# Optimization experiments

Hardware: AMD Instinct MI355X
Metric: run time of the kernel (lower is better)

## Reference

```python
import jax, jax.numpy as jnp
import numpy as np

INPUT_DIM = 10
SIG_DEPTH = 3
HIDDEN = 64
D_AUG = INPUT_DIM + 1  # time augmentation
LOGSIG_DIM = min(sum(D_AUG ** k // max(1, k) for k in range(1, SIG_DEPTH + 1)), 512)  # = 512
B, N = 1024, 256


def _compute_logsigs(features):
    """Vectorized computation of the per-step prefix-path signature features.

    For prefix length k+1 the torch code time-augments with linspace(0,1,k+1),
    i.e. dt = 1/k, which makes the time-related signature terms k-dependent.
    All terms reduce to cumulative sums over t, computed once for all k.
    Returns (B, N, LOGSIG_DIM); row k=0 is zeros (torch uses zeros at k=0).
    """
    Bsz, n, D = features.shape
    d = D + 1  # augmented dim (time first)
    dtype = features.dtype
    x0 = features[:, :1, :]
    inc = features[:, 1:, :] - features[:, :-1, :]          # (B, n-1, D) feature increments
    rel = features - x0                                      # x_t - x_0, (B, n, D)
    t_idx = jnp.arange(n - 1, dtype=dtype)
    # A[k-1] = sum_{t<k} t * dx_t   (time-row of level-2 term, before dt scaling)
    A = jnp.cumsum(t_idx[None, :, None] * inc, axis=1)       # (B, n-1, D)
    # Bc[k-1] = sum_{t=0}^{k-1} (x_t - x_0)   (time-column, before dt scaling)
    Bc = jnp.cumsum(rel[:, :-1, :], axis=1)                  # (B, n-1, D)
    # C[k-1] = sum_{t<k} (x_t - x_0) outer dx_t  (feature-feature level-2 block)
    C = jnp.cumsum(rel[:, :-1, :, None] * inc[:, :, None, :], axis=1)  # (B, n-1, D, D)
    ks = jnp.arange(1, n, dtype=dtype)                       # k = 1..n-1
    inv_k = 1.0 / ks
    tt = 0.5 * (ks - 1) * inv_k                              # sum t*dt^2 = (k-1)/(2k)
    # level-1: [T=1, x_k - x_0]
    sig1 = jnp.concatenate([jnp.ones((Bsz, n - 1, 1), dtype), rel[:, 1:, :]], axis=-1)  # (B, n-1, d)
    # level-2 matrix, augmented order [time, features]
    sig2 = jnp.zeros((Bsz, n - 1, d, d), dtype)
    sig2 = sig2.at[:, :, 0, 0].set(tt[None, :])
    sig2 = sig2.at[:, :, 0, 1:].set(inv_k[None, :, None] * A)
    sig2 = sig2.at[:, :, 1:, 0].set(inv_k[None, :, None] * Bc)
    sig2 = sig2.at[:, :, 1:, 1:].set(C)
    sig2f = sig2.reshape(Bsz, n - 1, d * d)
    # level-3 (torch: flatten(sig1 outer sig2_flat), truncated); only build needed rows
    sig3_len = LOGSIG_DIM - d - d * d                        # 512 - 11 - 121 = 380
    rows = (sig3_len + d * d - 1) // (d * d)                 # 4 rows of sig1 suffice
    sig3 = (sig1[..., :rows, None] * sig2f[..., None, :]).reshape(Bsz, n - 1, rows * d * d)[..., :sig3_len]
    logsig = jnp.concatenate([sig1, sig2f, sig3], axis=-1)[..., :LOGSIG_DIM]  # (B, n-1, 512)
    return jnp.concatenate([jnp.zeros((Bsz, 1, LOGSIG_DIM), dtype), logsig], axis=1)


def setup_inputs() -> dict:
    key = jax.random.key(0)
    k0, k1, k2, k3 = jax.random.split(key, 4)
    features = jax.random.normal(k0, (B, N, INPUT_DIM), jnp.float32)
    in_dim = LOGSIG_DIM + INPUT_DIM + 1  # 523
    W1 = jax.random.normal(k1, (in_dim, HIDDEN), jnp.float32) / np.sqrt(in_dim)
    b1 = jnp.zeros((HIDDEN,), jnp.float32)
    W2 = jax.random.normal(k2, (HIDDEN, HIDDEN), jnp.float32) / np.sqrt(HIDDEN)
    b2 = jnp.zeros((HIDDEN,), jnp.float32)
    W3 = jax.random.normal(k3, (HIDDEN, 1), jnp.float32) / np.sqrt(HIDDEN)
    b3 = jnp.zeros((1,), jnp.float32)
    return {"features": features, "W1": W1, "b1": b1, "W2": W2, "b2": b2, "W3": W3, "b3": b3}


def reference(features, W1, b1, W2, b2, W3, b3):
    logsigs = _compute_logsigs(features)  # (B, N, LOGSIG_DIM)
    Bsz = features.shape[0]

    def step(prev_delta, inputs):
        ls, ft = inputs  # (B, L), (B, D)
        x = jnp.concatenate([ls, ft, prev_delta], axis=-1)
        h = jax.nn.relu(x @ W1 + b1)
        h = jax.nn.relu(h @ W2 + b2)
        delta = h @ W3 + b3  # (B, 1)
        return delta, delta[:, 0]

    ls_t = jnp.swapaxes(logsigs, 0, 1)   # (N, B, L)
    ft_t = jnp.swapaxes(features, 0, 1)  # (N, B, D)
    _, deltas = jax.lax.scan(step, jnp.zeros((Bsz, 1), features.dtype), (ls_t, ft_t))
    return jnp.swapaxes(deltas, 0, 1)    # (B, N)
```

## Files before the change

### kernel.cpp

```cpp
#include <hip/hip_runtime.h>

#define NB 1024
#define NT 256
#define IND 10
#define HID 64

#define KSTEPS 14
#define XS 456
#define WMF_HALVES (KSTEPS * 4 * 64 * 8)

typedef short bf16x8 __attribute__((ext_vector_type(8)));
typedef float f32x4 __attribute__((ext_vector_type(4)));

__device__ __forceinline__ int qmap(int kk) {
    if (kk < 10) return 1 + kk;
    if (kk < 20) return 11 * (kk - 10 + 1);
    int i = (kk - 20) / 10, c = (kk - 20) % 10;
    return 11 * (i + 1) + 1 + c;
}

__device__ __forceinline__ unsigned bf16rne(float x) {
    unsigned u = __float_as_uint(x);
    return (u + 0x7fffu + ((u >> 16) & 1u)) >> 16;
}
__device__ __forceinline__ unsigned pk2(float a, float b) {
    return bf16rne(a) | (bf16rne(b) << 16);
}

__device__ float wm_value(int kk, int j, const float* __restrict__ W1,
                          const float* __restrict__ b1) {
    if (kk < 384) {
        int sec = kk >> 7;
        int rem = kk & 127;
        int w = rem >> 5, i = rem & 31;
        if (i >= 30) return 0.f;
        int q = qmap(30 * w + i);
        if (sec == 0) return W1[(11 + q) * 64 + j] + W1[(132 + q) * 64 + j];
        if (sec == 1) return W1[(253 + q) * 64 + j];
        return W1[(374 + q) * 64 + j];
    }
    if (kk < 400) {
        int i = kk - 384;
        if (i < 10) return W1[(496 + i) * 64 + j];
        if (i == 10) return W1[506 * 64 + j];
        return W1[(507 + (i - 11)) * 64 + j];
    }
    if (kk < 410) return W1[(1 + (kk - 400)) * 64 + j];
    if (kk < 420) return W1[(512 + (kk - 410)) * 64 + j];
    if (kk == 420) return W1[11 * 64 + j] + W1[132 * 64 + j];
    if (kk == 421) return W1[253 * 64 + j];
    if (kk == 422) return W1[374 * 64 + j];
    if (kk == 423) return W1[495 * 64 + j];
    if (kk == 424) return W1[0 * 64 + j];
    if (kk == 425) return b1[j];
    return 0.f;
}

__global__ void pack_mfma_kernel(const float* __restrict__ W1,
                                 const float* __restrict__ b1,
                                 unsigned short* __restrict__ Wmf) {
    int idx = blockIdx.x * 256 + threadIdx.x;
    if (idx >= WMF_HALVES) return;
    int half = idx & 7;
    int lane = (idx >> 3) & 63;
    int rec = idx >> 9;
    int s = rec >> 2, jb = rec & 3;
    int kk = 32 * s + (lane >> 4) * 8 + half;
    int j = 16 * jb + (lane & 15);
    Wmf[idx] = (unsigned short)bf16rne(wm_value(kk, j, W1, b1));
}

__global__ __launch_bounds__(256, 1) void presig9_kernel(
    const float* __restrict__ features, const unsigned short* __restrict__ Wmf,
    float* __restrict__ pre1) {
    const int b = blockIdx.x;
    const int tid = threadIdx.x;
    const int l = tid & 63;
    const int wu = tid >> 6;

    __shared__ __align__(16) float sF[NT * IND];
    __shared__ __align__(16) unsigned short sX[64 * XS];
    __shared__ float sBase[128];

    {
        const float4* src = (const float4*)(features + b * (NT * IND));
        float4* dst = (float4*)sF;
        for (int e = tid; e < NT * IND / 4; e += 256) dst[e] = src[e];
    }
    float f0[IND];
#pragma unroll
    for (int c = 0; c < IND; ++c) f0[c] = features[b * (NT * IND) + c];

    if (tid < 128) sBase[tid] = 0.f;
    __syncthreads();

    for (int tile = 0; tile < 4; ++tile) {
        const int t0 = tile * 64;

        const int r = t0 + l;
        float rf = (float)r;
        float fr[IND], rel[IND], inc[IND];
#pragma unroll
        for (int c = 0; c < IND; ++c) fr[c] = sF[r * IND + c];
#pragma unroll
        for (int c = 0; c < IND; ++c) rel[c] = fr[c] - f0[c];
        {
            bool last = (r >= NT - 1);
#pragma unroll
            for (int c = 0; c < IND; ++c)
                inc[c] = last ? 0.f : (sF[(r + 1) * IND + c] - fr[c]);
        }
        float p[30], own[30];
        if (wu == 0) {
#pragma unroll
            for (int c = 0; c < 10; ++c) p[c] = rf * inc[c];
#pragma unroll
            for (int i = 0; i < 10; ++i) p[10 + i] = rel[i];
#pragma unroll
            for (int c = 0; c < 10; ++c) p[20 + c] = rel[0] * inc[c];
        } else {
            const int i0 = 3 * wu - 2;
#pragma unroll
            for (int q = 0; q < 30; ++q) {
                int i = i0 + q / 10, c = q % 10;
                p[q] = rel[i] * inc[c];
            }
        }
#pragma unroll
        for (int i = 0; i < 30; ++i) own[i] = p[i];
#pragma unroll
        for (int dsh = 0; dsh < 6; ++dsh) {
            const int d = 1 << dsh;
            bool ok = (l >= d);
#pragma unroll
            for (int i = 0; i < 30; ++i) {
                float v = __shfl_up(p[i], d, 64);
                if (ok) p[i] += v;
            }
        }
        float inv_r = (r > 0) ? 1.f / rf : 0.f;
        float v[30];
#pragma unroll
        for (int i = 0; i < 30; ++i) {
            float x = sBase[wu * 32 + i] + p[i] - own[i];
            if (wu == 0 && i < 20) x *= inv_r;
            v[i] = x;
        }

        {
            float g0 = rel[0], g1 = rel[1];
            uint4* xr = (uint4*)&sX[l * XS];
            uint4* x0 = (uint4*)&sX[l * XS + 128];
            uint4* x1 = (uint4*)&sX[l * XS + 256];
            int qb = 8 * wu;
#pragma unroll
            for (int q = 0; q < 3; ++q) {
                uint4 tr, t0v, t1v;
                tr.x = pk2(v[8*q+0], v[8*q+1]); tr.y = pk2(v[8*q+2], v[8*q+3]);
                tr.z = pk2(v[8*q+4], v[8*q+5]); tr.w = pk2(v[8*q+6], v[8*q+7]);
                t0v.x = pk2(g0*v[8*q+0], g0*v[8*q+1]); t0v.y = pk2(g0*v[8*q+2], g0*v[8*q+3]);
                t0v.z = pk2(g0*v[8*q+4], g0*v[8*q+5]); t0v.w = pk2(g0*v[8*q+6], g0*v[8*q+7]);
                t1v.x = pk2(g1*v[8*q+0], g1*v[8*q+1]); t1v.y = pk2(g1*v[8*q+2], g1*v[8*q+3]);
                t1v.z = pk2(g1*v[8*q+4], g1*v[8*q+5]); t1v.w = pk2(g1*v[8*q+6], g1*v[8*q+7]);
                xr[wu * 4 + q] = tr; x0[wu * 4 + q] = t0v; x1[wu * 4 + q] = t1v;
            }
            {
                uint4 tr, t0v, t1v;
                tr.x = pk2(v[24], v[25]); tr.y = pk2(v[26], v[27]);
                tr.z = pk2(v[28], v[29]); tr.w = 0u;
                t0v.x = pk2(g0*v[24], g0*v[25]); t0v.y = pk2(g0*v[26], g0*v[27]);
                t0v.z = pk2(g0*v[28], g0*v[29]); t0v.w = 0u;
                t1v.x = pk2(g1*v[24], g1*v[25]); t1v.y = pk2(g1*v[26], g1*v[27]);
                t1v.z = pk2(g1*v[28], g1*v[29]); t1v.w = 0u;
                xr[wu * 4 + 3] = tr; x0[wu * 4 + 3] = t0v; x1[wu * 4 + 3] = t1v;
            }
            (void)qb;
        }
        if (wu == 0) {
            float g2 = rel[2];
            float ttv = 0.5f * (rf - 1.f) * inv_r;
            float gate = (r > 0) ? 1.f : 0.f;
            uint4* xe = (uint4*)&sX[l * XS + 384];
            uint4 u;
            u.x = pk2(g2*v[0], g2*v[1]);  u.y = pk2(g2*v[2], g2*v[3]);
            u.z = pk2(g2*v[4], g2*v[5]);  u.w = pk2(g2*v[6], g2*v[7]);
            xe[0] = u;
            u.x = pk2(g2*v[8], g2*v[9]);  u.y = pk2(g2*v[10], g2*v[20]);
            u.z = pk2(g2*v[21], g2*v[22]); u.w = pk2(g2*v[23], g2*v[24]);
            xe[1] = u;
            u.x = pk2(rel[0], rel[1]); u.y = pk2(rel[2], rel[3]);
            u.z = pk2(rel[4], rel[5]); u.w = pk2(rel[6], rel[7]);
            xe[2] = u;
            u.x = pk2(rel[8], rel[9]); u.y = pk2(fr[0], fr[1]);
            u.z = pk2(fr[2], fr[3]);   u.w = pk2(fr[4], fr[5]);
            xe[3] = u;
            u.x = pk2(fr[6], fr[7]); u.y = pk2(fr[8], fr[9]);
            u.z = pk2(ttv, ttv * rel[0]); u.w = pk2(ttv * rel[1], ttv * rel[2]);
            xe[4] = u;
            u.x = pk2(gate, 1.0f); u.y = 0u; u.z = 0u; u.w = 0u;
            xe[5] = u;
            u.x = 0u; u.y = 0u; u.z = 0u; u.w = 0u;
            xe[6] = u; xe[7] = u;
        }
        if (l == 63) {
#pragma unroll
            for (int i = 0; i < 30; ++i) sBase[wu * 32 + i] += p[i];
        }
        __syncthreads();

        {
            const int m = l & 15, quad = l >> 4;
            const unsigned short* arow = &sX[(16 * wu + m) * XS + 8 * quad];
            const bf16x8* bp = (const bf16x8*)Wmf;
            f32x4 ac0 = {0.f, 0.f, 0.f, 0.f}, ac1 = ac0, ac2 = ac0, ac3 = ac0;
#pragma unroll
            for (int s = 0; s < KSTEPS; ++s) {
                bf16x8 af = *(const bf16x8*)(arow + 32 * s);
                bf16x8 bf0 = bp[(s * 4 + 0) * 64 + l];
                bf16x8 bf1 = bp[(s * 4 + 1) * 64 + l];
                bf16x8 bf2 = bp[(s * 4 + 2) * 64 + l];
                bf16x8 bf3 = bp[(s * 4 + 3) * 64 + l];
                ac0 = __builtin_amdgcn_mfma_f32_16x16x32_bf16(af, bf0, ac0, 0, 0, 0);
                ac1 = __builtin_amdgcn_mfma_f32_16x16x32_bf16(af, bf1, ac1, 0, 0, 0);
                ac2 = __builtin_amdgcn_mfma_f32_16x16x32_bf16(af, bf2, ac2, 0, 0, 0);
                ac3 = __builtin_amdgcn_mfma_f32_16x16x32_bf16(af, bf3, ac3, 0, 0, 0);
            }
            float* op = pre1 + b * (NT * HID) + (t0 + 16 * wu) * HID + m;
            const int rowb = quad * 4;
#pragma unroll
            for (int reg = 0; reg < 4; ++reg) {
                op[(rowb + reg) * HID + 0]  = ac0[reg];
                op[(rowb + reg) * HID + 16] = ac1[reg];
                op[(rowb + reg) * HID + 32] = ac2[reg];
                op[(rowb + reg) * HID + 48] = ac3[reg];
            }
        }
        __syncthreads();
    }
}

template <int CTRL, int RMASK>
__device__ __forceinline__ float dpp_add(float x) {
    int v = __builtin_amdgcn_update_dpp(0, __float_as_int(x), CTRL, RMASK, 0xf, false);
    return x + __int_as_float(v);
}

#define W2_EACH(X) X(0) X(1) X(2) X(3) X(4) X(5) X(6) X(7) \
    X(8) X(9) X(10) X(11) X(12) X(13) X(14) X(15)

__global__ __launch_bounds__(64, 1) void scan_kernel(
    const float* __restrict__ pre1, const float* __restrict__ W1,
    const float* __restrict__ W2, const float* __restrict__ b2,
    const float* __restrict__ W3, const float* __restrict__ b3,
    float* __restrict__ out) {
    const int b = blockIdx.x;
    const int j = threadIdx.x;

    __shared__ __align__(16) float sH[64];

#define DECLW(q) float4 w2_##q = make_float4( \
        W2[(4*(q)+0)*64 + j], W2[(4*(q)+1)*64 + j], \
        W2[(4*(q)+2)*64 + j], W2[(4*(q)+3)*64 + j]);
    W2_EACH(DECLW)
#undef DECLW
    float w1l = W1[522 * 64 + j];
    float b2j = b2[j], w3j = W3[j], b3v = b3[0];

    const float* pb_ = pre1 + b * (NT * HID);
    float delta = 0.f;
    float outbuf = 0.f;

#define GEMVQ(q) { float4 h4 = *(const float4*)&sH[4*(q)]; \
        a0 = fmaf(h4.x, w2_##q.x, a0); a1 = fmaf(h4.y, w2_##q.y, a1); \
        a2 = fmaf(h4.z, w2_##q.z, a2); a3 = fmaf(h4.w, w2_##q.w, a3); }

#define SCAN_STEP(pv, mm) { \
        float h1 = fmaxf(fmaf(delta, w1l, (pv)), 0.f); \
        sH[j] = h1; \
        float a0 = 0.f, a1 = 0.f, a2 = 0.f, a3 = 0.f; \
        W2_EACH(GEMVQ) \
        float h2 = fmaxf((a0 + a1) + (a2 + a3) + b2j, 0.f); \
        float qv = h2 * w3j; \
        qv = dpp_add<0x111, 0xf>(qv); \
        qv = dpp_add<0x112, 0xf>(qv); \
        qv = dpp_add<0x114, 0xf>(qv); \
        qv = dpp_add<0x118, 0xf>(qv); \
        qv = dpp_add<0x142, 0xa>(qv); \
        qv = dpp_add<0x143, 0xc>(qv); \
        float tot = __uint_as_float(__builtin_amdgcn_readlane(__float_as_uint(qv), 63)); \
        delta = tot + b3v; \
        if (j == ((mm) & 63)) outbuf = delta; \
        if (((mm) & 63) == 63) out[b * NT + ((mm) & ~63) + j] = outbuf; }

    float r0 = pb_[0 * 64 + j], r1 = pb_[1 * 64 + j], r2 = pb_[2 * 64 + j],
          r3 = pb_[3 * 64 + j], r4 = pb_[4 * 64 + j], r5 = pb_[5 * 64 + j],
          r6 = pb_[6 * 64 + j], r7 = pb_[7 * 64 + j];
    for (int g = 0; g < NT; g += 8) {
        int nb = g + 8;
        float n0 = pb_[min(nb + 0, NT - 1) * 64 + j];
        float n1 = pb_[min(nb + 1, NT - 1) * 64 + j];
        float n2 = pb_[min(nb + 2, NT - 1) * 64 + j];
        float n3 = pb_[min(nb + 3, NT - 1) * 64 + j];
        float n4 = pb_[min(nb + 4, NT - 1) * 64 + j];
        float n5 = pb_[min(nb + 5, NT - 1) * 64 + j];
        float n6 = pb_[min(nb + 6, NT - 1) * 64 + j];
        float n7 = pb_[min(nb + 7, NT - 1) * 64 + j];
        SCAN_STEP(r0, g + 0)
        SCAN_STEP(r1, g + 1)
        SCAN_STEP(r2, g + 2)
        SCAN_STEP(r3, g + 3)
        SCAN_STEP(r4, g + 4)
        SCAN_STEP(r5, g + 5)
        SCAN_STEP(r6, g + 6)
        SCAN_STEP(r7, g + 7)
        r0 = n0; r1 = n1; r2 = n2; r3 = n3; r4 = n4; r5 = n5; r6 = n6; r7 = n7;
    }
#undef SCAN_STEP
#undef GEMVQ
}

__global__ __launch_bounds__(256) void logsig_hedge_fallback(
    const float* __restrict__ features, const float* __restrict__ W1,
    const float* __restrict__ b1, const float* __restrict__ W2,
    const float* __restrict__ b2, const float* __restrict__ W3,
    const float* __restrict__ b3, float* __restrict__ out) {
    const int b = blockIdx.x;
    const int tid = threadIdx.x;
    const int j = tid & 63;
    const int s = tid >> 6;

    __shared__ __align__(16) float sF[NT * IND];
    __shared__ __align__(16) float sSig[128];
    __shared__ float sA[IND], sB[IND], sC[IND * IND];
    __shared__ float sRel[IND];
    __shared__ __align__(16) float sPart[4 * 64];
    __shared__ __align__(16) float sH1[64];

    for (int idx = tid; idx < NT * IND; idx += 256)
        sF[idx] = features[b * (NT * IND) + idx];
    if (tid < 100) sC[tid] = 0.f;
    else if (tid < 110) sA[tid - 100] = 0.f;
    else if (tid < 120) sB[tid - 110] = 0.f;
    else if (tid >= 121 && tid < 128) sSig[tid] = 0.f;

    float vs[32], vb[32], vc[32];
#pragma unroll
    for (int mm = 0; mm < 32; ++mm) {
        int mp = 32 * s + mm;
        if (mp < 121) {
            vs[mm] = W1[(11 + mp) * 64 + j] + W1[(132 + mp) * 64 + j];
            vb[mm] = W1[(253 + mp) * 64 + j];
            vc[mm] = W1[(374 + mp) * 64 + j];
        } else { vs[mm] = 0.f; vb[mm] = 0.f; vc[mm] = 0.f; }
    }
    float ex[17];
#pragma unroll
    for (int q = 0; q < 17; ++q) ex[q] = 0.f;
    if (s == 1) {
#pragma unroll
        for (int q = 0; q < 11; ++q) ex[q] = W1[q * 64 + j];
    } else if (s == 2) {
#pragma unroll
        for (int q = 0; q < 10; ++q) ex[q] = W1[(512 + q) * 64 + j];
        ex[10] = b1[j];
    } else if (s == 3) {
#pragma unroll
        for (int q = 0; q < 17; ++q) ex[q] = W1[(495 + q) * 64 + j];
    }
    float w2p[16];
#pragma unroll
    for (int ii = 0; ii < 16; ++ii) w2p[ii] = W2[(16 * s + ii) * 64 + j];

    float w1l = 0.f, b2j = 0.f, w3j = 0.f, b3v = 0.f;
    if (s == 0) { w1l = W1[522 * 64 + j]; b2j = b2[j]; w3j = W3[j]; b3v = b3[0]; }
    float delta = 0.f;

    __syncthreads();

    for (int m = 0; m < NT; ++m) {
        if (m > 0) {
            if (tid < 100) {
                int i = tid / 10, c = tid % 10;
                float rp = sF[(m - 1) * 10 + i] - sF[i];
                float ic = sF[m * 10 + c] - sF[(m - 1) * 10 + c];
                sC[tid] += rp * ic;
            } else if (tid < 110) {
                int i = tid - 100;
                sA[i] += (float)(m - 1) * (sF[m * 10 + i] - sF[(m - 1) * 10 + i]);
            } else if (tid < 120) {
                int i = tid - 110;
                sB[i] += sF[(m - 1) * 10 + i] - sF[i];
            }
            __syncthreads();
            float inv_k = 1.0f / (float)m;
            if (tid == 0) sSig[0] = 0.5f * (float)(m - 1) * inv_k;
            else if (tid < 11) sSig[tid] = inv_k * sA[tid - 1];
            else if (tid < 121) {
                int i = tid / 11 - 1, c = tid % 11;
                sSig[tid] = (c == 0) ? inv_k * sB[i] : sC[i * 10 + (c - 1)];
            } else if (tid < 131) {
                int f = tid - 121;
                sRel[f] = sF[m * 10 + f] - sF[f];
            }
            __syncthreads();
        }
        float part = 0.f;
        if (m > 0) {
            float pa = 0.f, pb = 0.f, pc = 0.f;
#pragma unroll
            for (int q = 0; q < 8; ++q) {
                float4 sv = *(const float4*)&sSig[32 * s + 4 * q];
                pa = fmaf(sv.x, vs[4 * q + 0], pa);
                pb = fmaf(sv.x, vb[4 * q + 0], pb);
                pc = fmaf(sv.x, vc[4 * q + 0], pc);
                pa = fmaf(sv.y, vs[4 * q + 1], pa);
                pb = fmaf(sv.y, vb[4 * q + 1], pb);
                pc = fmaf(sv.y, vc[4 * q + 1], pc);
                pa = fmaf(sv.z, vs[4 * q + 2], pa);
                pb = fmaf(sv.z, vb[4 * q + 2], pb);
                pc = fmaf(sv.z, vc[4 * q + 2], pc);
                pa = fmaf(sv.w, vs[4 * q + 3], pa);
                pb = fmaf(sv.w, vb[4 * q + 3], pb);
                pc = fmaf(sv.w, vc[4 * q + 3], pc);
            }
            part = pa + sRel[0] * pb + sRel[1] * pc;
            if (s == 3) {
                float pd = 0.f;
#pragma unroll
                for (int q = 0; q < 17; ++q) pd = fmaf(sSig[q], ex[q], pd);
                part = fmaf(sRel[2], pd, part);
            }
            if (s == 1) {
                part += ex[0];
#pragma unroll
                for (int i = 0; i < 10; ++i) part = fmaf(sRel[i], ex[1 + i], part);
            }
        }
        if (s == 2) {
            float pf = ex[10];
#pragma unroll
            for (int f = 0; f < 10; ++f) pf = fmaf(sF[m * 10 + f], ex[f], pf);
            part += pf;
        }
        sPart[s * 64 + j] = part;
        __syncthreads();
        if (s == 0) {
            float x = sPart[j] + sPart[64 + j] + sPart[128 + j] + sPart[192 + j];
            sH1[j] = fmaxf(fmaf(delta, w1l, x), 0.f);
        }
        __syncthreads();
        {
            float hp = 0.f;
#pragma unroll
            for (int q = 0; q < 4; ++q) {
                float4 hv = *(const float4*)&sH1[16 * s + 4 * q];
                hp = fmaf(hv.x, w2p[4 * q + 0], hp);
                hp = fmaf(hv.y, w2p[4 * q + 1], hp);
                hp = fmaf(hv.z, w2p[4 * q + 2], hp);
                hp = fmaf(hv.w, w2p[4 * q + 3], hp);
            }
            sPart[s * 64 + j] = hp;
        }
        __syncthreads();
        if (s == 0) {
            float x2 = sPart[j] + sPart[64 + j] + sPart[128 + j] + sPart[192 + j] + b2j;
            float h2 = fmaxf(x2, 0.f);
            float dv = h2 * w3j;
#pragma unroll
            for (int off = 32; off > 0; off >>= 1) dv += __shfl_xor(dv, off, 64);
            delta = dv + b3v;
            if (j == 0) out[b * NT + m] = delta;
        }
        __syncthreads();
    }
}

extern "C" void kernel_launch(void* const* d_in, const int* in_sizes, int n_in,
                              void* d_out, int out_size, void* d_ws, size_t ws_size,
                              hipStream_t stream) {
    const float* features = (const float*)d_in[0];
    const float* W1 = (const float*)d_in[1];
    const float* b1 = (const float*)d_in[2];
    const float* W2 = (const float*)d_in[3];
    const float* b2 = (const float*)d_in[4];
    const float* W3 = (const float*)d_in[5];
    const float* b3 = (const float*)d_in[6];
    float* out = (float*)d_out;

    const size_t wmf_bytes = (size_t)WMF_HALVES * 2;
    const size_t w_pad     = ((wmf_bytes + 255) / 256) * 256;
    const size_t pre_bytes = (size_t)NB * NT * HID * sizeof(float);
    if (ws_size >= w_pad + pre_bytes) {
        unsigned short* Wmf = (unsigned short*)d_ws;
        float* pre1 = (float*)((char*)d_ws + w_pad);
        pack_mfma_kernel<<<(WMF_HALVES + 255) / 256, 256, 0, stream>>>(W1, b1, Wmf);
        presig9_kernel<<<NB, 256, 0, stream>>>(features, Wmf, pre1);
        scan_kernel<<<NB, 64, 0, stream>>>(pre1, W1, W2, b2, W3, b3, out);
    } else {
        logsig_hedge_fallback<<<NB, 256, 0, stream>>>(features, W1, b1, W2, b2, W3, b3, out);
    }
}
```

Baseline: 283.0 us.

## Split scan GEMV across four wavefronts with readlane broadcast and LDS reduction

The sequential scan kernel now runs 256 threads per batch row instead of 64. Each wavefront holds a 16-row slice of W2 and broadcasts h1 with readlane rather than round-tripping through LDS. Partial sums are combined through a double-buffered LDS array after a barrier. This shortens the per-step dependency chain of the 64x64 GEMV, at the cost of a block-wide barrier per step and redundant work across the four waves.

```diff
diff --git a/kernel.cpp b/kernel.cpp
--- a/kernel.cpp
+++ b/kernel.cpp
@@ -152,7 +152,6 @@
             uint4* xr = (uint4*)&sX[l * XS];
             uint4* x0 = (uint4*)&sX[l * XS + 128];
             uint4* x1 = (uint4*)&sX[l * XS + 256];
-            int qb = 8 * wu;
 #pragma unroll
             for (int q = 0; q < 3; ++q) {
                 uint4 tr, t0v, t1v;
@@ -174,7 +173,6 @@
                 t1v.z = pk2(g1*v[28], g1*v[29]); t1v.w = 0u;
                 xr[wu * 4 + 3] = tr; x0[wu * 4 + 3] = t0v; x1[wu * 4 + 3] = t1v;
             }
-            (void)qb;
         }
         if (wu == 0) {
             float g2 = rel[2];
@@ -245,24 +243,20 @@
     return x + __int_as_float(v);
 }
 
-#define W2_EACH(X) X(0) X(1) X(2) X(3) X(4) X(5) X(6) X(7) \
-    X(8) X(9) X(10) X(11) X(12) X(13) X(14) X(15)
-
-__global__ __launch_bounds__(64, 1) void scan_kernel(
+__global__ __launch_bounds__(256, 1) void scan4_kernel(
     const float* __restrict__ pre1, const float* __restrict__ W1,
     const float* __restrict__ W2, const float* __restrict__ b2,
     const float* __restrict__ W3, const float* __restrict__ b3,
     float* __restrict__ out) {
     const int b = blockIdx.x;
-    const int j = threadIdx.x;
-
-    __shared__ __align__(16) float sH[64];
-
-#define DECLW(q) float4 w2_##q = make_float4( \
-        W2[(4*(q)+0)*64 + j], W2[(4*(q)+1)*64 + j], \
-        W2[(4*(q)+2)*64 + j], W2[(4*(q)+3)*64 + j]);
-    W2_EACH(DECLW)
-#undef DECLW
+    const int j = threadIdx.x & 63;
+    const int w = __builtin_amdgcn_readfirstlane(threadIdx.x >> 6);
+
+    __shared__ __align__(16) float sPart[2][4 * 64];
+
+    float w2r[16];
+#pragma unroll
+    for (int ii = 0; ii < 16; ++ii) w2r[ii] = W2[(16 * w + ii) * 64 + j];
     float w1l = W1[522 * 64 + j];
     float b2j = b2[j], w3j = W3[j], b3v = b3[0];
 
@@ -270,16 +264,28 @@
     float delta = 0.f;
     float outbuf = 0.f;
 
-#define GEMVQ(q) { float4 h4 = *(const float4*)&sH[4*(q)]; \
-        a0 = fmaf(h4.x, w2_##q.x, a0); a1 = fmaf(h4.y, w2_##q.y, a1); \
-        a2 = fmaf(h4.z, w2_##q.z, a2); a3 = fmaf(h4.w, w2_##q.w, a3); }
-
-#define SCAN_STEP(pv, mm) { \
+#define SCAN_STEP4(pv, mm) { \
         float h1 = fmaxf(fmaf(delta, w1l, (pv)), 0.f); \
-        sH[j] = h1; \
+        float hb[16]; \
+        _Pragma("unroll") \
+        for (int ii = 0; ii < 16; ++ii) \
+            hb[ii] = __uint_as_float(__builtin_amdgcn_readlane( \
+                __float_as_uint(h1), 16 * w + ii)); \
         float a0 = 0.f, a1 = 0.f, a2 = 0.f, a3 = 0.f; \
-        W2_EACH(GEMVQ) \
-        float h2 = fmaxf((a0 + a1) + (a2 + a3) + b2j, 0.f); \
+        _Pragma("unroll") \
+        for (int q = 0; q < 4; ++q) { \
+            a0 = fmaf(w2r[4 * q + 0], hb[4 * q + 0], a0); \
+            a1 = fmaf(w2r[4 * q + 1], hb[4 * q + 1], a1); \
+            a2 = fmaf(w2r[4 * q + 2], hb[4 * q + 2], a2); \
+            a3 = fmaf(w2r[4 * q + 3], hb[4 * q + 3], a3); \
+        } \
+        sPart[(mm) & 1][w * 64 + j] = (a0 + a1) + (a2 + a3); \
+        asm volatile("s_waitcnt lgkmcnt(0)\n\ts_barrier" ::: "memory"); \
+        float p0 = sPart[(mm) & 1][j]; \
+        float p1 = sPart[(mm) & 1][64 + j]; \
+        float p2 = sPart[(mm) & 1][128 + j]; \
+        float p3 = sPart[(mm) & 1][192 + j]; \
+        float h2 = fmaxf((p0 + p1) + (p2 + p3) + b2j, 0.f); \
         float qv = h2 * w3j; \
         qv = dpp_add<0x111, 0xf>(qv); \
         qv = dpp_add<0x112, 0xf>(qv); \
@@ -289,8 +295,10 @@
         qv = dpp_add<0x143, 0xc>(qv); \
         float tot = __uint_as_float(__builtin_amdgcn_readlane(__float_as_uint(qv), 63)); \
         delta = tot + b3v; \
-        if (j == ((mm) & 63)) outbuf = delta; \
-        if (((mm) & 63) == 63) out[b * NT + ((mm) & ~63) + j] = outbuf; }
+        if (w == 0) { \
+            if (j == ((mm) & 63)) outbuf = delta; \
+            if (((mm) & 63) == 63) out[b * NT + ((mm) & ~63) + j] = outbuf; \
+        } }
 
     float r0 = pb_[0 * 64 + j], r1 = pb_[1 * 64 + j], r2 = pb_[2 * 64 + j],
           r3 = pb_[3 * 64 + j], r4 = pb_[4 * 64 + j], r5 = pb_[5 * 64 + j],
@@ -305,18 +313,17 @@
         float n5 = pb_[min(nb + 5, NT - 1) * 64 + j];
         float n6 = pb_[min(nb + 6, NT - 1) * 64 + j];
         float n7 = pb_[min(nb + 7, NT - 1) * 64 + j];
-        SCAN_STEP(r0, g + 0)
-        SCAN_STEP(r1, g + 1)
-        SCAN_STEP(r2, g + 2)
-        SCAN_STEP(r3, g + 3)
-        SCAN_STEP(r4, g + 4)
-        SCAN_STEP(r5, g + 5)
-        SCAN_STEP(r6, g + 6)
-        SCAN_STEP(r7, g + 7)
+        SCAN_STEP4(r0, g + 0)
+        SCAN_STEP4(r1, g + 1)
+        SCAN_STEP4(r2, g + 2)
+        SCAN_STEP4(r3, g + 3)
+        SCAN_STEP4(r4, g + 4)
+        SCAN_STEP4(r5, g + 5)
+        SCAN_STEP4(r6, g + 6)
+        SCAN_STEP4(r7, g + 7)
         r0 = n0; r1 = n1; r2 = n2; r3 = n3; r4 = n4; r5 = n5; r6 = n6; r7 = n7;
     }
-#undef SCAN_STEP
-#undef GEMVQ
+#undef SCAN_STEP4
 }
 
 __global__ __launch_bounds__(256) void logsig_hedge_fallback(
@@ -495,7 +502,7 @@
         float* pre1 = (float*)((char*)d_ws + w_pad);
         pack_mfma_kernel<<<(WMF_HALVES + 255) / 256, 256, 0, stream>>>(W1, b1, Wmf);
         presig9_kernel<<<NB, 256, 0, stream>>>(features, Wmf, pre1);
-        scan_kernel<<<NB, 64, 0, stream>>>(pre1, W1, W2, b2, W3, b3, out);
+        scan4_kernel<<<NB, 256, 0, stream>>>(pre1, W1, W2, b2, W3, b3, out);
     } else {
         logsig_hedge_fallback<<<NB, 256, 0, stream>>>(features, W1, b1, W2, b2, W3, b3, out);
     }
```

Result: slower. 326.6 us (+15.4%).
